# Optimization experiments

Measured on AMD Instinct MI355X. Metric: run time of the kernel, lower is better.

The kernel has to match this reference:

```python
import jax, jax.numpy as jnp
import numpy as np

B, T, C = 16, 512, 1024
D, K, W = 4096, 128, 8


def _scatter_topk(a, k, use_values):
    """Top-k along last axis; return dense array with top-k values (or 1.0) scattered, zeros elsewhere."""
    shp = a.shape
    a2 = a.reshape(-1, shp[-1])
    vals, idx = jax.lax.top_k(a2, k)
    rows = jnp.arange(a2.shape[0])[:, None]
    src = vals if use_values else jnp.ones_like(vals)
    return jnp.zeros_like(a2).at[rows, idx].set(src).reshape(shp)


def _window_topk(x, k, window_size):
    # x: (B, T, D)
    b, t, d = x.shape
    stride = max(1, window_size // 2)
    if stride >= t:
        num_windows, pad, t_pad = 1, 0, t
    else:
        num_windows = (t - window_size) // stride + 1
        required = (num_windows - 1) * stride + window_size
        pad = max(0, required - t)
        t_pad = t + pad
    if pad > 0:
        x = jnp.pad(x, ((0, 0), (0, pad), (0, 0)))
    starts = jnp.arange(num_windows) * stride                      # (NW,)
    tidx = starts[:, None] + jnp.arange(window_size)               # (NW, W)
    x_windows = x[:, tidx, :]                                      # (B, NW, W, D)
    window_sums = x_windows.sum(axis=2)                            # (B, NW, D)
    mask_windows = _scatter_topk(window_sums, k, use_values=False)  # (B, NW, D)
    votes = (x_windows * mask_windows[:, :, None, :]).reshape(b, num_windows * window_size, d)
    feature_votes = jnp.zeros((b, t_pad, d), x.dtype).at[:, tidx.reshape(-1)].add(votes)
    mask_combined = _scatter_topk(feature_votes, k, use_values=False)  # (B, Tp, D)
    x_sparse = x * mask_combined
    return x_sparse[:, :t - 0, :] if pad > 0 else x_sparse


def setup_inputs() -> dict:
    key = jax.random.key(0)
    ks = jax.random.split(key, 4)
    x_ssl = jax.random.normal(ks[0], (B, T, C), jnp.float32)
    W_dec = jax.random.normal(ks[1], (C, D), jnp.float32)
    W_dec = W_dec / jnp.linalg.norm(W_dec, axis=0, keepdims=True)
    W_enc = W_dec.T                                                # tied init, as in module
    W1 = jax.random.normal(ks[2], (256, D), jnp.float32) * (1.0 / np.sqrt(D))
    W2 = jax.random.normal(ks[3], (2, 256), jnp.float32) * (1.0 / np.sqrt(256))
    return dict(
        x_ssl=x_ssl, W_enc=W_enc, b_enc=jnp.zeros((D,), jnp.float32),
        W_dec=W_dec, b_dec=jnp.zeros((C,), jnp.float32),
        ln_g=jnp.ones((D,), jnp.float32), ln_b=jnp.zeros((D,), jnp.float32),
        W1=W1, b1=jnp.zeros((256,), jnp.float32),
        W2=W2, b2=jnp.zeros((2,), jnp.float32),
    )


def reference(x_ssl, W_enc, b_enc, W_dec, b_dec, ln_g, ln_b, W1, b1, W2, b2):
    b, t, c = x_ssl.shape
    x_flat = x_ssl.reshape(b * t, c)
    # SAE encode with window top-k (window_size=8 > 1 path)
    pre = jnp.einsum('nc,dc->nd', x_flat - b_dec, W_enc) + b_enc
    post_relu = jax.nn.relu(pre).reshape(b, t, -1)                 # (B, T, D)
    encoded = _window_topk(post_relu, K, W)                        # (B, T, D)
    encoded_flat = encoded.reshape(b * t, -1)
    # SAE decode + reconstruction loss
    x_recon = jnp.einsum('nd,cd->nc', encoded_flat, W_dec) + b_dec
    sae_loss = jnp.mean((x_recon - x_flat) ** 2)
    # classifier on pooled sparse features (dropout is inference no-op)
    pooled = encoded.mean(axis=1)                                  # (B, D) == AdaptiveAvgPool1d(1)
    mu = pooled.mean(axis=-1, keepdims=True)
    var = pooled.var(axis=-1, keepdims=True)
    ln = (pooled - mu) / jnp.sqrt(var + 1e-5) * ln_g + ln_b
    h = jax.nn.relu(ln @ W1.T + b1)
    logits = h @ W2.T + b2
    log_probs = jax.nn.log_softmax(logits, axis=-1)
    return log_probs, sae_loss
```

## Files before the change

kernel.cpp:

```cpp
#include <hip/hip_runtime.h>

#define BB   16
#define TT   512
#define CC   1024
#define DD   4096
#define NN   (BB*TT)
#define NWIN 127
#define KTOP 128

typedef __attribute__((ext_vector_type(8))) short short8;
typedef _Float16 half8 __attribute__((ext_vector_type(8)));
typedef __attribute__((ext_vector_type(4))) float f32x4;

__device__ __forceinline__ unsigned short f2bf(float f) {
    unsigned u = __float_as_uint(f);
    unsigned r = (u + 0x7fffu + ((u >> 16) & 1u)) >> 16;
    return (unsigned short)r;
}
__device__ __forceinline__ float bf2f(unsigned x) {
    return __uint_as_float((x & 0xffffu) << 16);
}
__device__ __forceinline__ unsigned short f2h(float f) {
    union { _Float16 h; unsigned short u; } c;
    c.h = (_Float16)f;
    return c.u;
}
__device__ __forceinline__ unsigned tokey(float f) {
    unsigned u = __float_as_uint(f);
    return (u & 0x80000000u) ? ~u : (u | 0x80000000u);
}
__device__ __forceinline__ void async_lds16(const void* g, void* l) {
    __builtin_amdgcn_global_load_lds((const __attribute__((address_space(1))) void*)g,
                                     (__attribute__((address_space(3))) void*)l, 16, 0, 0);
}

__device__ __forceinline__ unsigned wave_prefix_incl(unsigned v) {
    int lane = threadIdx.x & 63;
#pragma unroll
    for (int off = 1; off < 64; off <<= 1) {
        unsigned n = __shfl_up(v, off, 64);
        if (lane >= off) v += n;
    }
    return v;
}
__device__ __forceinline__ unsigned wave_suffix_incl(unsigned v) {
    int lane = threadIdx.x & 63;
#pragma unroll
    for (int off = 1; off < 64; off <<= 1) {
        unsigned n = __shfl_down(v, off, 64);
        if (lane + off < 64) v += n;
    }
    return v;
}

__device__ __forceinline__ unsigned select_top128(const unsigned* keys,
                                                  unsigned* hist, unsigned* shx) {
    const int tid = threadIdx.x, wid = tid >> 6, lane = tid & 63;
    const unsigned ZKEY = 0x80000000u;
    unsigned cpos = 0, cz = 0;
#pragma unroll
    for (int i = 0; i < 16; ++i) {
        cpos += (keys[i] > ZKEY);
        cz   += (keys[i] == ZKEY);
    }
    unsigned ppos = wave_prefix_incl(cpos);
    unsigned pz   = wave_prefix_incl(cz);
    if (lane == 63) { shx[wid] = ppos; shx[4 + wid] = pz; }
    __syncthreads();
    unsigned nz = shx[0] + shx[1] + shx[2] + shx[3];
    unsigned selbits = 0u;
    if (nz <= KTOP) {
        unsigned need = KTOP - nz;
        unsigned zr = pz - cz;
        if (wid > 0) zr += shx[4];
        if (wid > 1) zr += shx[5];
        if (wid > 2) zr += shx[6];
#pragma unroll
        for (int i = 0; i < 16; ++i) {
            bool sel = (keys[i] > ZKEY) || (keys[i] == ZKEY && zr < need);
            if (keys[i] == ZKEY) ++zr;
            selbits |= (sel ? 1u : 0u) << i;
        }
        return selbits;
    }
    unsigned k2[16];
#pragma unroll
    for (int i = 0; i < 16; ++i) k2[i] = (keys[i] > ZKEY) ? keys[i] : 0u;
    unsigned prefix = 0u, pmask = 0u, Kr = KTOP;
    for (int shift = 24; shift >= 0; shift -= 8) {
        hist[tid] = 0u; hist[256 + tid] = 0u; hist[512 + tid] = 0u; hist[768 + tid] = 0u;
        __syncthreads();
        unsigned* h = hist + (wid << 8);
#pragma unroll
        for (int i = 0; i < 16; ++i)
            if (k2[i] && (k2[i] & pmask) == prefix) atomicAdd(&h[(k2[i] >> shift) & 255u], 1u);
        __syncthreads();
        unsigned v = hist[tid] + hist[256 + tid] + hist[512 + tid] + hist[768 + tid];
        unsigned s = wave_suffix_incl(v);
        if (lane == 0) shx[wid] = s;
        __syncthreads();
        unsigned stot = s;
        if (wid == 0) stot += shx[1] + shx[2] + shx[3];
        else if (wid == 1) stot += shx[2] + shx[3];
        else if (wid == 2) stot += shx[3];
        unsigned above = stot - v;
        if (stot >= Kr && above < Kr) { shx[8] = (unsigned)tid; shx[9] = Kr - above; }
        __syncthreads();
        prefix |= shx[8] << shift;
        pmask |= 0xFFu << shift;
        Kr = shx[9];
    }
    unsigned T = prefix, need = Kr;
    unsigned ce = 0;
#pragma unroll
    for (int i = 0; i < 16; ++i) ce += (k2[i] == T);
    unsigned pe = wave_prefix_incl(ce);
    __syncthreads();
    if (lane == 63) shx[4 + wid] = pe;
    __syncthreads();
    unsigned er = pe - ce;
    if (wid > 0) er += shx[4];
    if (wid > 1) er += shx[5];
    if (wid > 2) er += shx[6];
#pragma unroll
    for (int i = 0; i < 16; ++i) {
        bool sel = (k2[i] > T) || (k2[i] == T && er < need);
        if (k2[i] == T) ++er;
        selbits |= (sel ? 1u : 0u) << i;
    }
    return selbits;
}

__global__ __launch_bounds__(256) void k_convert_all(const float* __restrict__ x,
                                                     const float* __restrict__ Wenc,
                                                     const float* __restrict__ Wdec,
                                                     const float* __restrict__ bdec,
                                                     unsigned short* __restrict__ xh,
                                                     unsigned short* __restrict__ wh,
                                                     unsigned short* __restrict__ wdb) {
    const int bid = blockIdx.x;
    if (bid < 8192) {
        size_t i = (size_t)bid * 256 + threadIdx.x;
        float4 v = ((const float4*)x)[i];
        size_t c = (i * 4) & (CC - 1);
        v.x -= bdec[c]; v.y -= bdec[c + 1]; v.z -= bdec[c + 2]; v.w -= bdec[c + 3];
        uint2 o;
        o.x = (unsigned)f2h(v.x) | ((unsigned)f2h(v.y) << 16);
        o.y = (unsigned)f2h(v.z) | ((unsigned)f2h(v.w) << 16);
        ((uint2*)xh)[i] = o;
    } else if (bid < 12288) {
        size_t i = (size_t)(bid - 8192) * 256 + threadIdx.x;
        float4 v = ((const float4*)Wenc)[i];
        uint2 o;
        o.x = (unsigned)f2h(v.x) | ((unsigned)f2h(v.y) << 16);
        o.y = (unsigned)f2h(v.z) | ((unsigned)f2h(v.w) << 16);
        ((uint2*)wh)[i] = o;
    } else {
        size_t i = (size_t)(bid - 12288) * 256 + threadIdx.x;
        float4 v = ((const float4*)Wdec)[i];
        uint2 o;
        o.x = (unsigned)f2bf(v.x) | ((unsigned)f2bf(v.y) << 16);
        o.y = (unsigned)f2bf(v.z) | ((unsigned)f2bf(v.w) << 16);
        ((uint2*)wdb)[i] = o;
    }
}

__device__ __forceinline__ void stage_tile_swz(const unsigned short* gbase, size_t ldk,
                                               unsigned short* lds, int wave, int lane) {
    const int sub = lane >> 3;
    const int cj  = (lane & 7) ^ sub;
#pragma unroll
    for (int i = 0; i < 4; ++i) {
        int n = wave * 4 + i;
        int r = n * 8 + sub;
        async_lds16(gbase + (size_t)r * ldk + cj * 8, lds + n * 512);
    }
}

__global__ __launch_bounds__(256) void k_gemm_enc_f16(const unsigned short* __restrict__ Ah,
                                                      const unsigned short* __restrict__ Bh,
                                                      const float* __restrict__ bias,
                                                      float* __restrict__ Cout,
                                                      float* __restrict__ gsum,
                                                      int Ndim, int Kdim) {
    __shared__ __align__(16) unsigned short smem[2 * 128 * 64];
    unsigned short* At = smem;
    unsigned short* Bt = smem + 128 * 64;
    float* cbuf = (float*)smem;
    const int tid = threadIdx.x, wave = tid >> 6, lane = tid & 63;
    const int bm = blockIdx.y * 128, bn = blockIdx.x * 128;
    const int wm = (wave >> 1) * 64, wn = (wave & 1) * 64;
    const int rA = lane & 15, q8 = (lane >> 4) * 8, rp7 = rA & 7;
    const int q = lane >> 4, qr = q * 4, cl = lane & 15;
    f32x4 acc[4][4] = {};
    for (int k0 = 0; k0 < Kdim; k0 += 64) {
        __syncthreads();
        stage_tile_swz(Ah + (size_t)bm * Kdim + k0, Kdim, At, wave, lane);
        stage_tile_swz(Bh + (size_t)bn * Kdim + k0, Kdim, Bt, wave, lane);
        __syncthreads();
#pragma unroll
        for (int kk = 0; kk < 64; kk += 32) {
            const int sc = ((((kk + q8) >> 3) ^ rp7) << 3);
            half8 a[4], b[4];
#pragma unroll
            for (int mt = 0; mt < 4; ++mt) a[mt] = *(const half8*)(At + (wm + mt * 16 + rA) * 64 + sc);
#pragma unroll
            for (int nt = 0; nt < 4; ++nt) b[nt] = *(const half8*)(Bt + (wn + nt * 16 + rA) * 64 + sc);
#pragma unroll
            for (int mt = 0; mt < 4; ++mt)
#pragma unroll
                for (int nt = 0; nt < 4; ++nt)
                    acc[mt][nt] = __builtin_amdgcn_mfma_f32_16x16x32_f16(a[mt], b[nt], acc[mt][nt], 0, 0, 0);
        }
    }
    float bv[4];
#pragma unroll
    for (int nt = 0; nt < 4; ++nt) bv[nt] = bias[bn + wn + nt * 16 + cl];
#pragma unroll
    for (int p = 0; p < 2; ++p) {
        __syncthreads();
        if ((wave >> 1) == p) {
#pragma unroll
            for (int nt = 0; nt < 4; ++nt) {
                int lc = wn + nt * 16 + cl;
                int pcb = (lc >> 2) ^ (q << 1);
#pragma unroll
                for (int mt = 0; mt < 4; ++mt) {
#pragma unroll
                    for (int r = 0; r < 4; ++r) {
                        int lr = mt * 16 + qr + r;
                        float v = acc[mt][nt][r] + bv[nt];
                        v = v > 0.f ? v : 0.f;
                        cbuf[lr * 128 + pcb * 4 + (lc & 3)] = v;
                    }
                }
            }
        }
        __syncthreads();
#pragma unroll
        for (int i = 0; i < 2; ++i) {
            int gidx = i * 256 + tid;
            int grow = gidx >> 5;
            int colg = gidx & 31;
            float4 s = make_float4(0.f, 0.f, 0.f, 0.f);
#pragma unroll
            for (int j = 0; j < 4; ++j) {
                int lr = grow * 4 + j;
                int pcr = colg ^ (((lr >> 2) & 3) << 1);
                float4 v = *(const float4*)&cbuf[lr * 128 + pcr * 4];
                s.x += v.x; s.y += v.y; s.z += v.z; s.w += v.w;
                *(float4*)&Cout[(size_t)(bm + p * 64 + lr) * Ndim + bn + colg * 4] = v;
            }
            if (gsum)
                *(float4*)&gsum[(size_t)((bm >> 2) + p * 16 + grow) * Ndim + bn + colg * 4] = s;
        }
    }
}

__global__ __launch_bounds__(256) void k_gemm_recon(const unsigned short* __restrict__ A,
                                                    size_t lda,
                                                    const unsigned short* __restrict__ Bm,
                                                    const float* __restrict__ bdec,
                                                    const float* __restrict__ X,
                                                    float* __restrict__ sae,
                                                    int Ndim, int Kdim) {
    __shared__ __align__(16) unsigned short At[2][128 * 64];
    __shared__ __align__(16) unsigned short Bt[2][128 * 64];
    __shared__ float red[256];
    const int tid = threadIdx.x, wave = tid >> 6, lane = tid & 63;
    const int bm = blockIdx.y * 128, bn = blockIdx.x * 128;
    const int wm = (wave >> 1) * 64, wn = (wave & 1) * 64;
    const int rA = lane & 15, q8 = (lane >> 4) * 8, rp7 = rA & 7;
    f32x4 acc[4][4] = {};
    stage_tile_swz(A + (size_t)bm * lda, lda, At[0], wave, lane);
    stage_tile_swz(Bm + (size_t)bn * Kdim, Kdim, Bt[0], wave, lane);
    __syncthreads();
    for (int k0 = 0; k0 < Kdim; k0 += 64) {
        const int cur = (k0 >> 6) & 1;
        if (k0 + 64 < Kdim) {
            stage_tile_swz(A + (size_t)bm * lda + k0 + 64, lda, At[cur ^ 1], wave, lane);
            stage_tile_swz(Bm + (size_t)bn * Kdim + k0 + 64, Kdim, Bt[cur ^ 1], wave, lane);
        }
#pragma unroll
        for (int kk = 0; kk < 64; kk += 32) {
            const int sc = ((((kk + q8) >> 3) ^ rp7) << 3);
            short8 a[4], b[4];
#pragma unroll
            for (int mt = 0; mt < 4; ++mt) a[mt] = *(const short8*)(At[cur] + (wm + mt * 16 + rA) * 64 + sc);
#pragma unroll
            for (int nt = 0; nt < 4; ++nt) b[nt] = *(const short8*)(Bt[cur] + (wn + nt * 16 + rA) * 64 + sc);
#pragma unroll
            for (int mt = 0; mt < 4; ++mt)
#pragma unroll
                for (int nt = 0; nt < 4; ++nt)
                    acc[mt][nt] = __builtin_amdgcn_mfma_f32_16x16x32_bf16(a[mt], b[nt], acc[mt][nt], 0, 0, 0);
        }
        __syncthreads();
    }
    const int cl = lane & 15, qr = (lane >> 4) * 4;
    float lsum = 0.f;
#pragma unroll
    for (int nt = 0; nt < 4; ++nt) {
        int col = bn + wn + nt * 16 + cl;
        float bv = bdec[col];
#pragma unroll
        for (int mt = 0; mt < 4; ++mt) {
            int row0 = bm + wm + mt * 16 + qr;
#pragma unroll
            for (int r = 0; r < 4; ++r) {
                float v = acc[mt][nt][r] + bv - X[(size_t)(row0 + r) * Ndim + col];
                lsum += v * v;
            }
        }
    }
    red[tid] = lsum;
    __syncthreads();
    for (int s = 128; s > 0; s >>= 1) { if (tid < s) red[tid] += red[tid + s]; __syncthreads(); }
    if (tid == 0) atomicAdd(sae, red[0]);
}

__global__ __launch_bounds__(256) void k_winsum_g(const float* __restrict__ gsum,
                                                  unsigned* __restrict__ wmask) {
    __shared__ unsigned hist[1024];
    __shared__ unsigned shx[16];
    __shared__ unsigned short halves[256];
    const int tid = threadIdx.x, w = blockIdx.x, b = blockIdx.y;
    const float* g0 = gsum + ((size_t)(b * 128 + w)) * DD + tid * 16;
    const float* g1 = g0 + DD;
    unsigned keys[16];
#pragma unroll
    for (int q = 0; q < 4; ++q) {
        float4 u = *(const float4*)(g0 + q * 4);
        float4 v = *(const float4*)(g1 + q * 4);
        keys[q * 4 + 0] = tokey(u.x + v.x);
        keys[q * 4 + 1] = tokey(u.y + v.y);
        keys[q * 4 + 2] = tokey(u.z + v.z);
        keys[q * 4 + 3] = tokey(u.w + v.w);
    }
    unsigned selbits = select_top128(keys, hist, shx);
    halves[tid] = (unsigned short)selbits;
    __syncthreads();
    if (tid < 128)
        wmask[(size_t)(b * NWIN + w) * 128 + tid] =
            (unsigned)halves[2 * tid] | ((unsigned)halves[2 * tid + 1] << 16);
}

__global__ __launch_bounds__(256) void k_winsum_p(const float* __restrict__ post,
                                                  unsigned* __restrict__ wmask) {
    __shared__ unsigned hist[1024];
    __shared__ unsigned shx[16];
    __shared__ unsigned short halves[256];
    const int tid = threadIdx.x, w = blockIdx.x, b = blockIdx.y;
    const float* base = post + (size_t)(b * TT + w * 4) * DD + tid * 16;
    float s[16] = {};
#pragma unroll
    for (int j = 0; j < 8; ++j) {
        const float* rp = base + (size_t)j * DD;
#pragma unroll
        for (int q = 0; q < 4; ++q) {
            float4 u = *(const float4*)(rp + q * 4);
            s[q * 4 + 0] += u.x; s[q * 4 + 1] += u.y; s[q * 4 + 2] += u.z; s[q * 4 + 3] += u.w;
        }
    }
    unsigned keys[16];
#pragma unroll
    for (int i = 0; i < 16; ++i) keys[i] = tokey(s[i]);
    unsigned selbits = select_top128(keys, hist, shx);
    halves[tid] = (unsigned short)selbits;
    __syncthreads();
    if (tid < 128)
        wmask[(size_t)(b * NWIN + w) * 128 + tid] =
            (unsigned)halves[2 * tid] | ((unsigned)halves[2 * tid + 1] << 16);
}

__global__ __launch_bounds__(256) void k_votes(float* __restrict__ post,
                                               const unsigned* __restrict__ wmask,
                                               float* __restrict__ pooled) {
    __shared__ unsigned hist[1024];
    __shared__ unsigned shx[16];
    const int tid = threadIdx.x, t = blockIdx.x, b = blockIdx.y;
    float* rp = post + (size_t)(b * TT + t) * DD;
    int w1 = t >> 2, w0 = w1 - 1;
    unsigned mw0 = 0u, mw1 = 0u;
    if (w0 >= 0)        mw0 = wmask[(size_t)(b * NWIN + w0) * 128 + (tid >> 1)];
    if (w1 <= NWIN - 1) mw1 = wmask[(size_t)(b * NWIN + w1) * 128 + (tid >> 1)];
    const int bbase = (tid & 1) * 16;
    float vals[16];
    unsigned keys[16];
#pragma unroll
    for (int q = 0; q < 4; ++q) {
        float4 u = *(const float4*)(rp + tid * 16 + q * 4);
        vals[q * 4 + 0] = u.x; vals[q * 4 + 1] = u.y; vals[q * 4 + 2] = u.z; vals[q * 4 + 3] = u.w;
    }
#pragma unroll
    for (int i = 0; i < 16; ++i) {
        float cov = (float)(((mw0 >> (bbase + i)) & 1u) + ((mw1 >> (bbase + i)) & 1u));
        keys[i] = tokey(vals[i] * cov);
    }
    unsigned selbits = select_top128(keys, hist, shx);
    unsigned packed[8];
#pragma unroll
    for (int i = 0; i < 16; i += 2) {
        float v0 = (selbits >> i) & 1u ? vals[i] : 0.f;
        float v1 = (selbits >> (i + 1)) & 1u ? vals[i + 1] : 0.f;
        if (v0 != 0.f) atomicAdd(&pooled[(size_t)b * DD + tid * 16 + i], v0);
        if (v1 != 0.f) atomicAdd(&pooled[(size_t)b * DD + tid * 16 + i + 1], v1);
        packed[i >> 1] = (unsigned)f2bf(v0) | ((unsigned)f2bf(v1) << 16);
    }
    unsigned short* op = (unsigned short*)rp;
    *(uint4*)(op + tid * 16)     = *(uint4*)&packed[0];
    *(uint4*)(op + tid * 16 + 8) = *(uint4*)&packed[4];
}

__device__ __forceinline__ float block_sum(float v, float* red) {
    const int tid = threadIdx.x;
    red[tid] = v;
    __syncthreads();
    for (int s = 128; s > 0; s >>= 1) { if (tid < s) red[tid] += red[tid + s]; __syncthreads(); }
    float r = red[0];
    __syncthreads();
    return r;
}

__global__ __launch_bounds__(256) void k_head_ln(const float* __restrict__ pooled,
                                                 const float* __restrict__ lng,
                                                 const float* __restrict__ lnb,
                                                 float* __restrict__ lnout) {
    __shared__ float red[256];
    const int b = blockIdx.x, tid = threadIdx.x;
    float pv[16];
    float s = 0.f;
#pragma unroll
    for (int q = 0; q < 4; ++q) {
        float4 u = *(const float4*)(pooled + (size_t)b * DD + tid * 16 + q * 4);
        pv[q * 4 + 0] = u.x * (1.f / TT); pv[q * 4 + 1] = u.y * (1.f / TT);
        pv[q * 4 + 2] = u.z * (1.f / TT); pv[q * 4 + 3] = u.w * (1.f / TT);
        s += pv[q * 4 + 0] + pv[q * 4 + 1] + pv[q * 4 + 2] + pv[q * 4 + 3];
    }
    float mean = block_sum(s, red) * (1.f / (float)DD);
    float vs = 0.f;
#pragma unroll
    for (int i = 0; i < 16; ++i) { float c = pv[i] - mean; vs += c * c; }
    float var = block_sum(vs, red) * (1.f / (float)DD);
    float inv = rsqrtf(var + 1e-5f);
#pragma unroll
    for (int q = 0; q < 4; ++q) {
        float4 g = *(const float4*)(lng + tid * 16 + q * 4);
        float4 bb = *(const float4*)(lnb + tid * 16 + q * 4);
        float4 o;
        o.x = (pv[q * 4 + 0] - mean) * inv * g.x + bb.x;
        o.y = (pv[q * 4 + 1] - mean) * inv * g.y + bb.y;
        o.z = (pv[q * 4 + 2] - mean) * inv * g.z + bb.z;
        o.w = (pv[q * 4 + 3] - mean) * inv * g.w + bb.w;
        *(float4*)(lnout + (size_t)b * DD + tid * 16 + q * 4) = o;
    }
}

__global__ __launch_bounds__(256) void k_head_mlp(const float* __restrict__ lnout,
                                                  const float* __restrict__ W1,
                                                  const float* __restrict__ b1,
                                                  float* __restrict__ h) {
    const int gw = (blockIdx.x * 256 + threadIdx.x) >> 6;
    const int lane = threadIdx.x & 63;
    const int b = gw >> 8, row = gw & 255;
    const float* lp = lnout + (size_t)b * DD;
    const float* wr = W1 + (size_t)row * DD;
    float a = 0.f;
#pragma unroll
    for (int k = 0; k < DD / 64; ++k)
        a += lp[lane + 64 * k] * wr[lane + 64 * k];
#pragma unroll
    for (int off = 32; off > 0; off >>= 1) a += __shfl_down(a, off, 64);
    if (lane == 0) h[b * 256 + row] = fmaxf(a + b1[row], 0.f);
}

__global__ __launch_bounds__(256) void k_head_out(const float* __restrict__ h,
                                                  const float* __restrict__ W2,
                                                  const float* __restrict__ b2,
                                                  const float* __restrict__ sae,
                                                  float* __restrict__ out) {
    __shared__ float red[256];
    const int b = blockIdx.x, tid = threadIdx.x;
    float hv = h[b * 256 + tid];
    float l0 = block_sum(hv * W2[tid], red) + b2[0];
    float l1 = block_sum(hv * W2[256 + tid], red) + b2[1];
    if (tid == 0) {
        float m = fmaxf(l0, l1);
        float lse = m + logf(expf(l0 - m) + expf(l1 - m));
        out[2 * b] = l0 - lse;
        out[2 * b + 1] = l1 - lse;
        if (b == 0) out[32] = sae[0] * (1.f / (float)((size_t)NN * CC));
    }
}

extern "C" void kernel_launch(void* const* d_in, const int* in_sizes, int n_in,
                              void* d_out, int out_size, void* d_ws, size_t ws_size,
                              hipStream_t stream) {
    const float* x    = (const float*)d_in[0];
    const float* Wenc = (const float*)d_in[1];
    const float* benc = (const float*)d_in[2];
    const float* Wdec = (const float*)d_in[3];
    const float* bdec = (const float*)d_in[4];
    const float* lng  = (const float*)d_in[5];
    const float* lnb  = (const float*)d_in[6];
    const float* W1   = (const float*)d_in[7];
    const float* b1   = (const float*)d_in[8];
    const float* W2   = (const float*)d_in[9];
    const float* b2   = (const float*)d_in[10];
    float* out = (float*)d_out;

    char* ws = (char*)d_ws;
    float*          post  = (float*)(ws + 0);
    unsigned short* xh16  = (unsigned short*)(ws + 134217728);
    unsigned short* scr   = (unsigned short*)(ws + 150994944);
    unsigned short* wh16  = (unsigned short*)(ws + 167772160);
    unsigned short* wdecb = (unsigned short*)(ws + 184549376);
    unsigned*       wmask = (unsigned*)(ws + 192937984);
    float*          pooled= (float*)(ws + 193978368);
    float*          sae   = (float*)(ws + 194240512);
    float*          gsum  = (float*)(ws + 194240768);
    const bool use_gsum = ws_size >= (size_t)194240768 + 33554432;
    float* gptr = use_gsum ? gsum : nullptr;
    float* lnout = (float*)xh16;
    float* hbuf  = (float*)scr;

    hipMemsetAsync(pooled, 0, 262144 + 256, stream);

    k_convert_all<<<dim3(16384), 256, 0, stream>>>(x, Wenc, Wdec, bdec, xh16, wh16, wdecb);

    k_gemm_enc_f16<<<dim3(DD / 128, NN / 128), 256, 0, stream>>>(xh16, wh16, benc, post, gptr, DD, CC);
    if (use_gsum)
        k_winsum_g<<<dim3(NWIN, BB), 256, 0, stream>>>(gsum, wmask);
    else
        k_winsum_p<<<dim3(NWIN, BB), 256, 0, stream>>>(post, wmask);
    k_votes<<<dim3(TT, BB), 256, 0, stream>>>(post, wmask, pooled);
    k_gemm_recon<<<dim3(CC / 128, NN / 128), 256, 0, stream>>>((const unsigned short*)post, (size_t)2 * DD,
                                                               wdecb, bdec, x, sae, CC, DD);
    k_head_ln<<<dim3(BB), 256, 0, stream>>>(pooled, lng, lnb, lnout);
    k_head_mlp<<<dim3(1024), 256, 0, stream>>>(lnout, W1, b1, hbuf);
    k_head_out<<<dim3(BB), 256, 0, stream>>>(hbuf, W2, b2, sae, out);
}
```

Measured before the change: 454.0 us.

## Single-buffer recon GEMM LDS and batch eight tokens per votes block

The reconstruction GEMM drops its double-buffered LDS staging and uses one buffer with a barrier before and after each load, which halves LDS use so more blocks can share a CU, at the cost of losing the overlap between loading and computing. The votes kernel now handles eight timesteps per block and accumulates the pooled partial sums in registers, issuing one set of atomics per block instead of one per token. This cuts atomic traffic into the pooled buffer and the number of launched blocks, but serialises eight top-k selections inside each block.

```diff
diff --git a/kernel.cpp b/kernel.cpp
--- a/kernel.cpp
+++ b/kernel.cpp
@@ -264,38 +264,33 @@
                                                     const float* __restrict__ X,
                                                     float* __restrict__ sae,
                                                     int Ndim, int Kdim) {
-    __shared__ __align__(16) unsigned short At[2][128 * 64];
-    __shared__ __align__(16) unsigned short Bt[2][128 * 64];
+    __shared__ __align__(16) unsigned short At[128 * 64];
+    __shared__ __align__(16) unsigned short Bt[128 * 64];
     __shared__ float red[256];
     const int tid = threadIdx.x, wave = tid >> 6, lane = tid & 63;
     const int bm = blockIdx.y * 128, bn = blockIdx.x * 128;
     const int wm = (wave >> 1) * 64, wn = (wave & 1) * 64;
     const int rA = lane & 15, q8 = (lane >> 4) * 8, rp7 = rA & 7;
     f32x4 acc[4][4] = {};
-    stage_tile_swz(A + (size_t)bm * lda, lda, At[0], wave, lane);
-    stage_tile_swz(Bm + (size_t)bn * Kdim, Kdim, Bt[0], wave, lane);
-    __syncthreads();
     for (int k0 = 0; k0 < Kdim; k0 += 64) {
-        const int cur = (k0 >> 6) & 1;
-        if (k0 + 64 < Kdim) {
-            stage_tile_swz(A + (size_t)bm * lda + k0 + 64, lda, At[cur ^ 1], wave, lane);
-            stage_tile_swz(Bm + (size_t)bn * Kdim + k0 + 64, Kdim, Bt[cur ^ 1], wave, lane);
-        }
+        __syncthreads();
+        stage_tile_swz(A + (size_t)bm * lda + k0, lda, At, wave, lane);
+        stage_tile_swz(Bm + (size_t)bn * Kdim + k0, Kdim, Bt, wave, lane);
+        __syncthreads();
 #pragma unroll
         for (int kk = 0; kk < 64; kk += 32) {
             const int sc = ((((kk + q8) >> 3) ^ rp7) << 3);
             short8 a[4], b[4];
 #pragma unroll
-            for (int mt = 0; mt < 4; ++mt) a[mt] = *(const short8*)(At[cur] + (wm + mt * 16 + rA) * 64 + sc);
-#pragma unroll
-            for (int nt = 0; nt < 4; ++nt) b[nt] = *(const short8*)(Bt[cur] + (wn + nt * 16 + rA) * 64 + sc);
+            for (int mt = 0; mt < 4; ++mt) a[mt] = *(const short8*)(At + (wm + mt * 16 + rA) * 64 + sc);
+#pragma unroll
+            for (int nt = 0; nt < 4; ++nt) b[nt] = *(const short8*)(Bt + (wn + nt * 16 + rA) * 64 + sc);
 #pragma unroll
             for (int mt = 0; mt < 4; ++mt)
 #pragma unroll
                 for (int nt = 0; nt < 4; ++nt)
                     acc[mt][nt] = __builtin_amdgcn_mfma_f32_16x16x32_bf16(a[mt], b[nt], acc[mt][nt], 0, 0, 0);
         }
-        __syncthreads();
     }
     const int cl = lane & 15, qr = (lane >> 4) * 4;
     float lsum = 0.f;
@@ -373,43 +368,52 @@
             (unsigned)halves[2 * tid] | ((unsigned)halves[2 * tid + 1] << 16);
 }
 
-__global__ __launch_bounds__(256) void k_votes(float* __restrict__ post,
-                                               const unsigned* __restrict__ wmask,
-                                               float* __restrict__ pooled) {
+__global__ __launch_bounds__(256) void k_votes8(float* __restrict__ post,
+                                                const unsigned* __restrict__ wmask,
+                                                float* __restrict__ pooled) {
     __shared__ unsigned hist[1024];
     __shared__ unsigned shx[16];
-    const int tid = threadIdx.x, t = blockIdx.x, b = blockIdx.y;
-    float* rp = post + (size_t)(b * TT + t) * DD;
-    int w1 = t >> 2, w0 = w1 - 1;
-    unsigned mw0 = 0u, mw1 = 0u;
-    if (w0 >= 0)        mw0 = wmask[(size_t)(b * NWIN + w0) * 128 + (tid >> 1)];
-    if (w1 <= NWIN - 1) mw1 = wmask[(size_t)(b * NWIN + w1) * 128 + (tid >> 1)];
+    const int tid = threadIdx.x, b = blockIdx.y;
+    const int t0 = blockIdx.x * 8;
     const int bbase = (tid & 1) * 16;
-    float vals[16];
-    unsigned keys[16];
-#pragma unroll
-    for (int q = 0; q < 4; ++q) {
-        float4 u = *(const float4*)(rp + tid * 16 + q * 4);
-        vals[q * 4 + 0] = u.x; vals[q * 4 + 1] = u.y; vals[q * 4 + 2] = u.z; vals[q * 4 + 3] = u.w;
-    }
-#pragma unroll
-    for (int i = 0; i < 16; ++i) {
-        float cov = (float)(((mw0 >> (bbase + i)) & 1u) + ((mw1 >> (bbase + i)) & 1u));
-        keys[i] = tokey(vals[i] * cov);
-    }
-    unsigned selbits = select_top128(keys, hist, shx);
-    unsigned packed[8];
-#pragma unroll
-    for (int i = 0; i < 16; i += 2) {
-        float v0 = (selbits >> i) & 1u ? vals[i] : 0.f;
-        float v1 = (selbits >> (i + 1)) & 1u ? vals[i + 1] : 0.f;
-        if (v0 != 0.f) atomicAdd(&pooled[(size_t)b * DD + tid * 16 + i], v0);
-        if (v1 != 0.f) atomicAdd(&pooled[(size_t)b * DD + tid * 16 + i + 1], v1);
-        packed[i >> 1] = (unsigned)f2bf(v0) | ((unsigned)f2bf(v1) << 16);
-    }
-    unsigned short* op = (unsigned short*)rp;
-    *(uint4*)(op + tid * 16)     = *(uint4*)&packed[0];
-    *(uint4*)(op + tid * 16 + 8) = *(uint4*)&packed[4];
+    float psum[16] = {};
+    for (int tt = 0; tt < 8; ++tt) {
+        const int t = t0 + tt;
+        float* rp = post + (size_t)(b * TT + t) * DD;
+        int w1 = t >> 2, w0 = w1 - 1;
+        unsigned mw0 = 0u, mw1 = 0u;
+        if (w0 >= 0)        mw0 = wmask[(size_t)(b * NWIN + w0) * 128 + (tid >> 1)];
+        if (w1 <= NWIN - 1) mw1 = wmask[(size_t)(b * NWIN + w1) * 128 + (tid >> 1)];
+        float vals[16];
+        unsigned keys[16];
+#pragma unroll
+        for (int q = 0; q < 4; ++q) {
+            float4 u = *(const float4*)(rp + tid * 16 + q * 4);
+            vals[q * 4 + 0] = u.x; vals[q * 4 + 1] = u.y; vals[q * 4 + 2] = u.z; vals[q * 4 + 3] = u.w;
+        }
+#pragma unroll
+        for (int i = 0; i < 16; ++i) {
+            float cov = (float)(((mw0 >> (bbase + i)) & 1u) + ((mw1 >> (bbase + i)) & 1u));
+            keys[i] = tokey(vals[i] * cov);
+        }
+        unsigned selbits = select_top128(keys, hist, shx);
+        unsigned packed[8];
+#pragma unroll
+        for (int i = 0; i < 16; i += 2) {
+            float v0 = (selbits >> i) & 1u ? vals[i] : 0.f;
+            float v1 = (selbits >> (i + 1)) & 1u ? vals[i + 1] : 0.f;
+            psum[i] += v0;
+            psum[i + 1] += v1;
+            packed[i >> 1] = (unsigned)f2bf(v0) | ((unsigned)f2bf(v1) << 16);
+        }
+        unsigned short* op = (unsigned short*)rp;
+        *(uint4*)(op + tid * 16)     = *(uint4*)&packed[0];
+        *(uint4*)(op + tid * 16 + 8) = *(uint4*)&packed[4];
+        __syncthreads();
+    }
+#pragma unroll
+    for (int i = 0; i < 16; ++i)
+        if (psum[i] != 0.f) atomicAdd(&pooled[(size_t)b * DD + tid * 16 + i], psum[i]);
 }
 
 __device__ __forceinline__ float block_sum(float v, float* red) {
@@ -533,7 +537,7 @@
         k_winsum_g<<<dim3(NWIN, BB), 256, 0, stream>>>(gsum, wmask);
     else
         k_winsum_p<<<dim3(NWIN, BB), 256, 0, stream>>>(post, wmask);
-    k_votes<<<dim3(TT, BB), 256, 0, stream>>>(post, wmask, pooled);
+    k_votes8<<<dim3(TT / 8, BB), 256, 0, stream>>>(post, wmask, pooled);
     k_gemm_recon<<<dim3(CC / 128, NN / 128), 256, 0, stream>>>((const unsigned short*)post, (size_t)2 * DD,
                                                                wdecb, bdec, x, sae, CC, DD);
     k_head_ln<<<dim3(BB), 256, 0, stream>>>(pooled, lng, lnb, lnout);
```

Measured after the change: 476.9 us. +5.0%, slower.
